# Kernel optimization log

Hardware: AMD Instinct MI355X
Metric: run time of the kernel (lower is better)

Reference implementation:

```python
import jax, jax.numpy as jnp
import numpy as np

N, D, H, E, K = 8192, 1024, 4096, 8, 2


def setup_inputs() -> dict:
    key = jax.random.key(0)
    ks = jax.random.split(key, 4)
    scaled = lambda k, shp, fan: (jax.random.normal(k, shp, jnp.float32) / np.sqrt(fan).astype(np.float32))
    return {
        "x": jax.random.normal(ks[0], (N, D), jnp.float32),
        "Wg": scaled(ks[1], (D, E), D),
        "bg": jnp.zeros((E,), jnp.float32),
        "W1": scaled(ks[2], (E, D, H), D),
        "b1": jnp.zeros((E, H), jnp.float32),
        "W2": scaled(ks[3], (E, H, D), H),
        "b2": jnp.zeros((E, D), jnp.float32),
    }


def reference(x, Wg, bg, W1, b1, W2, b2):
    # Gating: softmax over experts, top-k selection, renormalize top-k probs.
    gate_probs = jax.nn.softmax(x @ Wg + bg, axis=-1)            # [N, E]
    topk_p, topk_i = jax.lax.top_k(gate_probs, K)                # [N, K]
    topk_p = topk_p / topk_p.sum(axis=-1, keepdims=True)
    onehot = jax.nn.one_hot(topk_i, E, dtype=x.dtype)            # [N, K, E]
    # Per-token combine weight for each expert (0 if expert not in top-k).
    w = (onehot * topk_p[..., None]).sum(axis=1)                 # [N, E]

    out = jnp.zeros_like(x)
    for e in range(E):  # fixed small loop over structurally distinct experts
        h = jax.nn.relu(x @ W1[e] + b1[e])                       # dropout = identity (eval)
        out = out + w[:, e:e + 1] * (h @ W2[e] + b2[e])

    # Load-balancing auxiliary loss.
    importance = gate_probs.sum(axis=0)
    importance = importance / importance.sum()
    load = onehot.sum(axis=(0, 1)) / (x.shape[0] * K)            # [E]
    lb_loss = E * (importance * load).sum()
    return out, lb_loss
```

## Files before the change

kernel.cpp:

```cpp
#include <hip/hip_runtime.h>
#include <hip/hip_bf16.h>
#include <math.h>

#define NTOK 8192
#define DDIM 1024
#define HDIM 4096
#define NEXP 8
#define KTOP 2
#define MAXROWS 17408
#define MAXTILES 136

typedef __bf16 bf16x8 __attribute__((ext_vector_type(8)));
typedef float f32x4 __attribute__((ext_vector_type(4)));

#define GAS __attribute__((address_space(1)))
#define LAS __attribute__((address_space(3)))

__device__ __forceinline__ void async16(const void* g, void* l) {
  __builtin_amdgcn_global_load_lds((GAS void*)g, (LAS void*)l, 16, 0, 0);
}

#define XB_OFF     ((size_t)0)
#define W1T_OFF    (XB_OFF + (size_t)NTOK*DDIM*2)
#define ROWOUT_OFF W1T_OFF
#define W2T_OFF    (W1T_OFF + (size_t)NEXP*DDIM*HDIM*2)
#define HB_OFF     (W2T_OFF + (size_t)NEXP*HDIM*DDIM*2)
#define ROWTOK_OFF (HB_OFF + (size_t)MAXROWS*HDIM*2)
#define ROWW_OFF   (ROWTOK_OFF + (size_t)MAXROWS*4)
#define TOKE_OFF   (ROWW_OFF + (size_t)MAXROWS*4)
#define TOKW_OFF   (TOKE_OFF + (size_t)NTOK*KTOP*4)
#define TOKROW_OFF (TOKW_OFF + (size_t)NTOK*KTOP*4)
#define TILEE_OFF  (TOKROW_OFF + (size_t)NTOK*KTOP*4)
#define CNT_OFF    (TILEE_OFF + (size_t)256*4)
#define POS_OFF    (CNT_OFF + 64)
#define IMP_OFF    (POS_OFF + 64)
#define META_OFF   (IMP_OFF + 64)

__global__ void init_kernel(int* counts, float* importance) {
  if (threadIdx.x < NEXP) { counts[threadIdx.x] = 0; importance[threadIdx.x] = 0.f; }
}

__global__ void cast_x_kernel(const float* __restrict__ src, __hip_bfloat16* __restrict__ dst) {
  size_t i = ((size_t)blockIdx.x * blockDim.x + threadIdx.x) * 4;
  if (i < (size_t)NTOK * DDIM) {
    float4 v = *(const float4*)(src + i);
    dst[i + 0] = __float2bfloat16(v.x);
    dst[i + 1] = __float2bfloat16(v.y);
    dst[i + 2] = __float2bfloat16(v.z);
    dst[i + 3] = __float2bfloat16(v.w);
  }
}

__global__ __launch_bounds__(256) void transpose_cast_kernel(
    const float* __restrict__ src, __hip_bfloat16* __restrict__ dst, int R, int C) {
  __shared__ float tile[64][65];
  const int e = blockIdx.z;
  const float* s = src + (size_t)e * R * C;
  __hip_bfloat16* d = dst + (size_t)e * R * C;
  const int c0 = blockIdx.x * 64, r0 = blockIdx.y * 64;
  const int tc = (threadIdx.x & 15) * 4;
  const int tr = threadIdx.x >> 4;
#pragma unroll
  for (int p = 0; p < 4; ++p) {
    float4 v = *(const float4*)&s[(size_t)(r0 + tr + p * 16) * C + c0 + tc];
    tile[tr + p * 16][tc + 0] = v.x;
    tile[tr + p * 16][tc + 1] = v.y;
    tile[tr + p * 16][tc + 2] = v.z;
    tile[tr + p * 16][tc + 3] = v.w;
  }
  __syncthreads();
  const int oc = threadIdx.x >> 4;
  const int orr = (threadIdx.x & 15) * 4;
#pragma unroll
  for (int p = 0; p < 4; ++p) {
    const int c = oc + p * 16;
    __hip_bfloat16 tmp[4];
    tmp[0] = __float2bfloat16(tile[orr + 0][c]);
    tmp[1] = __float2bfloat16(tile[orr + 1][c]);
    tmp[2] = __float2bfloat16(tile[orr + 2][c]);
    tmp[3] = __float2bfloat16(tile[orr + 3][c]);
    *(ushort4*)&d[(size_t)(c0 + c) * R + r0 + orr] = *(ushort4*)tmp;
  }
}

__global__ __launch_bounds__(256) void gating_kernel(
    const float* __restrict__ x, const float* __restrict__ Wg, const float* __restrict__ bg,
    int* __restrict__ tok_e, float* __restrict__ tok_w,
    int* __restrict__ counts, float* __restrict__ importance) {
  const int tid = threadIdx.x, wid = tid >> 6, lane = tid & 63;
  const int t = blockIdx.x * 32 + wid * 8 + (lane >> 3);
  const int e = lane & 7;
  const float* xr = x + (size_t)t * DDIM;
  double dot = 0.0;
  for (int d = 0; d < DDIM; d += 4) {
    float4 xv = *(const float4*)(xr + d);
    dot += (double)xv.x * (double)Wg[(d + 0) * NEXP + e];
    dot += (double)xv.y * (double)Wg[(d + 1) * NEXP + e];
    dot += (double)xv.z * (double)Wg[(d + 2) * NEXP + e];
    dot += (double)xv.w * (double)Wg[(d + 3) * NEXP + e];
  }
  double logit = dot + (double)bg[e];
  double m = logit;
  for (int off = 1; off < 8; off <<= 1) {
    double o = __shfl_xor(m, off, 64);
    m = o > m ? o : m;
  }
  double p = exp(logit - m);
  double s = p;
  for (int off = 1; off < 8; off <<= 1) s += __shfl_xor(s, off, 64);
  float prob = (float)(p / s);

  __shared__ float imp[NEXP];
  __shared__ int cnt[NEXP];
  if (tid < NEXP) { imp[tid] = 0.f; cnt[tid] = 0; }
  __syncthreads();
  atomicAdd(&imp[e], prob);

  float bp = prob; int be = e;
  for (int off = 1; off < 8; off <<= 1) {
    float op = __shfl_xor(bp, off, 64); int oe = __shfl_xor(be, off, 64);
    if (op > bp || (op == bp && oe < be)) { bp = op; be = oe; }
  }
  float p2 = (e == be) ? -1.f : prob;
  float sp = p2; int se = e;
  for (int off = 1; off < 8; off <<= 1) {
    float op = __shfl_xor(sp, off, 64); int oe = __shfl_xor(se, off, 64);
    if (op > sp || (op == sp && oe < se)) { sp = op; se = oe; }
  }
  if (e == 0) {
    float tsum = bp + sp;
    tok_e[t * 2 + 0] = be; tok_e[t * 2 + 1] = se;
    tok_w[t * 2 + 0] = bp / tsum; tok_w[t * 2 + 1] = sp / tsum;
    atomicAdd(&cnt[be], 1); atomicAdd(&cnt[se], 1);
  }
  __syncthreads();
  if (tid < NEXP) {
    atomicAdd(&counts[tid], cnt[tid]);
    atomicAdd(&importance[tid], imp[tid]);
  }
}

__global__ void offsets_kernel(const int* __restrict__ counts, int* pos, int* tile_expert,
                               int* meta, int* row_token) {
  if (threadIdx.x == 0) {
    int pb = 0, tb = 0;
    for (int e = 0; e < NEXP; e++) {
      pos[e] = pb;
      int tiles = (counts[e] + 127) >> 7;
      for (int tt = 0; tt < tiles; ++tt) tile_expert[tb + tt] = e;
      pb += tiles * 128; tb += tiles;
    }
    meta[0] = tb;
  }
  __syncthreads();
  for (int i = threadIdx.x; i < MAXROWS; i += blockDim.x) row_token[i] = -1;
}

__global__ void scatter_kernel(const int* __restrict__ tok_e, const float* __restrict__ tok_w,
                               int* __restrict__ pos, int* __restrict__ row_token,
                               float* __restrict__ row_weight, int* __restrict__ tok_row) {
  __shared__ int lcnt[NEXP], lbase[NEXP];
  const int t = blockIdx.x * 256 + threadIdx.x;
  if (threadIdx.x < NEXP) lcnt[threadIdx.x] = 0;
  __syncthreads();
  const int e0 = tok_e[t * 2 + 0], e1 = tok_e[t * 2 + 1];
  const int s0 = atomicAdd(&lcnt[e0], 1);
  const int s1 = atomicAdd(&lcnt[e1], 1);
  __syncthreads();
  if (threadIdx.x < NEXP) lbase[threadIdx.x] = atomicAdd(&pos[threadIdx.x], lcnt[threadIdx.x]);
  __syncthreads();
  int r0 = lbase[e0] + s0; row_token[r0] = t; row_weight[r0] = tok_w[t * 2 + 0]; tok_row[t * 2 + 0] = r0;
  int r1 = lbase[e1] + s1; row_token[r1] = t; row_weight[r1] = tok_w[t * 2 + 1]; tok_row[t * 2 + 1] = r1;
}

__global__ __launch_bounds__(256) void gemm1_kernel(
    const __hip_bfloat16* __restrict__ xb, const __hip_bfloat16* __restrict__ w1t,
    const float* __restrict__ b1, __hip_bfloat16* __restrict__ hb,
    const int* __restrict__ row_token, const int* __restrict__ tile_expert,
    const int* __restrict__ meta) {
  const int tile_y = blockIdx.y;
  if (tile_y >= meta[0]) return;
  const int n0 = blockIdx.x * 128;
  const int e = tile_expert[tile_y];
  const int r0 = tile_y * 128;
  const int tid = threadIdx.x;
  const int wid = tid >> 6, lane = tid & 63;

  __shared__ __align__(16) __hip_bfloat16 As[2][128 * 32];
  __shared__ __align__(16) __hip_bfloat16 Bs[2][128 * 32];

  const int srow = wid * 32 + (lane >> 2);
  const int g = (((lane & 3) - (srow & 3) - ((srow >> 2) & 3)) & 3) * 8;
  int t0 = row_token[r0 + srow];      if (t0 < 0) t0 = 0;
  int t1 = row_token[r0 + srow + 16]; if (t1 < 0) t1 = 0;
  const __hip_bfloat16* ga0 = xb + (size_t)t0 * DDIM + g;
  const __hip_bfloat16* ga1 = xb + (size_t)t1 * DDIM + g;
  const __hip_bfloat16* gb0 = w1t + ((size_t)e * HDIM + n0 + srow) * DDIM + g;
  const __hip_bfloat16* gb1 = gb0 + (size_t)16 * DDIM;
  const int ldsA0 = (wid * 32) * 32, ldsA1 = (wid * 32 + 16) * 32;

  f32x4 acc[4][4] = {};
  const int wm = (wid & 1) * 64, wn = (wid >> 1) * 64;
  const int fr = lane & 15;
  const int soff = (((lane >> 4) + (lane & 3) + ((lane >> 2) & 3)) & 3) * 8;

#define STAGE1(b) do { \
    async16(ga0, &As[b][ldsA0]); async16(ga1, &As[b][ldsA1]); \
    async16(gb0, &Bs[b][ldsA0]); async16(gb1, &Bs[b][ldsA1]); \
    ga0 += 32; ga1 += 32; gb0 += 32; gb1 += 32; } while (0)

  STAGE1(0);
  for (int kt = 0; kt < DDIM / 32; ++kt) {
    const int cur = kt & 1;
    __syncthreads();
    if (kt + 1 < DDIM / 32) { if (cur) STAGE1(0); else STAGE1(1); }
    bf16x8 av[4], bv[4];
#pragma unroll
    for (int i = 0; i < 4; i++) av[i] = *(const bf16x8*)&As[cur][(wm + i * 16 + fr) * 32 + soff];
#pragma unroll
    for (int j = 0; j < 4; j++) bv[j] = *(const bf16x8*)&Bs[cur][(wn + j * 16 + fr) * 32 + soff];
#pragma unroll
    for (int i = 0; i < 4; i++)
#pragma unroll
      for (int j = 0; j < 4; j++)
        acc[i][j] = __builtin_amdgcn_mfma_f32_16x16x32_bf16(av[i], bv[j], acc[i][j], 0, 0, 0);
  }
#undef STAGE1

  const int crow = (lane >> 4) * 4;
  const int ccol = lane & 15;
#pragma unroll
  for (int j = 0; j < 4; j++) {
    const int gc = n0 + wn + j * 16 + ccol;
    const float bias = b1[e * HDIM + gc];
#pragma unroll
    for (int i = 0; i < 4; i++) {
      const int grb = r0 + wm + i * 16 + crow;
#pragma unroll
      for (int r = 0; r < 4; r++) {
        float v = acc[i][j][r] + bias;
        v = v > 0.f ? v : 0.f;
        hb[(size_t)(grb + r) * HDIM + gc] = __float2bfloat16(v);
      }
    }
  }
}

__global__ __launch_bounds__(256) void gemm2_kernel(
    const __hip_bfloat16* __restrict__ hb, const __hip_bfloat16* __restrict__ w2t,
    const float* __restrict__ b2, __hip_bfloat16* __restrict__ rowout,
    const int* __restrict__ tile_expert, const int* __restrict__ meta) {
  const int tile_y = blockIdx.x >> 3;
  const int cx = blockIdx.x & 7;
  if (tile_y >= meta[0]) return;
  const int n0 = cx * 128;
  const int e = tile_expert[tile_y];
  const int r0 = tile_y * 128;
  const int tid = threadIdx.x;
  const int wid = tid >> 6, lane = tid & 63;

  __shared__ __align__(16) __hip_bfloat16 As[2][128 * 32];
  __shared__ __align__(16) __hip_bfloat16 Bs[2][128 * 32];

  const int srow = wid * 32 + (lane >> 2);
  const int g = (((lane & 3) - (srow & 3) - ((srow >> 2) & 3)) & 3) * 8;
  const __hip_bfloat16* ga0 = hb + ((size_t)r0 + srow) * HDIM + g;
  const __hip_bfloat16* ga1 = ga0 + (size_t)16 * HDIM;
  const __hip_bfloat16* gb0 = w2t + ((size_t)e * DDIM + n0 + srow) * HDIM + g;
  const __hip_bfloat16* gb1 = gb0 + (size_t)16 * HDIM;
  const int ldsA0 = (wid * 32) * 32, ldsA1 = (wid * 32 + 16) * 32;

  f32x4 acc[4][4] = {};
  const int wm = (wid & 1) * 64, wn = (wid >> 1) * 64;
  const int fr = lane & 15;
  const int soff = (((lane >> 4) + (lane & 3) + ((lane >> 2) & 3)) & 3) * 8;

#define STAGE2(b) do { \
    async16(ga0, &As[b][ldsA0]); async16(ga1, &As[b][ldsA1]); \
    async16(gb0, &Bs[b][ldsA0]); async16(gb1, &Bs[b][ldsA1]); \
    ga0 += 32; ga1 += 32; gb0 += 32; gb1 += 32; } while (0)

  STAGE2(0);
  for (int kt = 0; kt < HDIM / 32; ++kt) {
    const int cur = kt & 1;
    __syncthreads();
    if (kt + 1 < HDIM / 32) { if (cur) STAGE2(0); else STAGE2(1); }
    bf16x8 av[4], bv[4];
#pragma unroll
    for (int i = 0; i < 4; i++) av[i] = *(const bf16x8*)&As[cur][(wm + i * 16 + fr) * 32 + soff];
#pragma unroll
    for (int j = 0; j < 4; j++) bv[j] = *(const bf16x8*)&Bs[cur][(wn + j * 16 + fr) * 32 + soff];
#pragma unroll
    for (int i = 0; i < 4; i++)
#pragma unroll
      for (int j = 0; j < 4; j++)
        acc[i][j] = __builtin_amdgcn_mfma_f32_16x16x32_bf16(av[i], bv[j], acc[i][j], 0, 0, 0);
  }
#undef STAGE2

  const int crow = (lane >> 4) * 4;
  const int ccol = lane & 15;
#pragma unroll
  for (int j = 0; j < 4; j++) {
    const int gc = n0 + wn + j * 16 + ccol;
    const float bias = b2[e * DDIM + gc];
#pragma unroll
    for (int i = 0; i < 4; i++) {
      const int rr = r0 + wm + i * 16 + crow;
#pragma unroll
      for (int r = 0; r < 4; r++)
        rowout[(size_t)(rr + r) * DDIM + gc] = __float2bfloat16(acc[i][j][r] + bias);
    }
  }
}

__global__ __launch_bounds__(256) void combine_kernel(
    const __hip_bfloat16* __restrict__ rowout, const int* __restrict__ tok_row,
    const float* __restrict__ row_weight, float* __restrict__ out) {
  const int idx = blockIdx.x * 256 + threadIdx.x;
  const int t = idx >> 7;
  const int d = (idx & 127) * 8;
  const int r0 = tok_row[t * 2 + 0], r1 = tok_row[t * 2 + 1];
  const float w0 = row_weight[r0], w1 = row_weight[r1];
  bf16x8 a = *(const bf16x8*)&rowout[(size_t)r0 * DDIM + d];
  bf16x8 b = *(const bf16x8*)&rowout[(size_t)r1 * DDIM + d];
  float o[8];
#pragma unroll
  for (int k = 0; k < 8; k++) o[k] = w0 * (float)a[k] + w1 * (float)b[k];
  float* dst = out + (size_t)t * DDIM + d;
  *(float4*)(dst + 0) = make_float4(o[0], o[1], o[2], o[3]);
  *(float4*)(dst + 4) = make_float4(o[4], o[5], o[6], o[7]);
}

__global__ void finalize_kernel(const float* __restrict__ importance,
                                const int* __restrict__ counts, float* __restrict__ lb_out) {
  if (threadIdx.x == 0 && blockIdx.x == 0) {
    float s = 0.f;
    for (int e = 0; e < NEXP; e++) s += importance[e];
    float lb = 0.f;
    for (int e = 0; e < NEXP; e++)
      lb += (importance[e] / s) * ((float)counts[e] / (float)(NTOK * KTOP));
    lb_out[0] = (float)NEXP * lb;
  }
}

extern "C" void kernel_launch(void* const* d_in, const int* in_sizes, int n_in,
                              void* d_out, int out_size, void* d_ws, size_t ws_size,
                              hipStream_t stream) {
  (void)in_sizes; (void)n_in; (void)out_size; (void)ws_size;
  const float* x  = (const float*)d_in[0];
  const float* Wg = (const float*)d_in[1];
  const float* bg = (const float*)d_in[2];
  const float* W1 = (const float*)d_in[3];
  const float* b1 = (const float*)d_in[4];
  const float* W2 = (const float*)d_in[5];
  const float* b2 = (const float*)d_in[6];
  float* out = (float*)d_out;

  char* ws = (char*)d_ws;
  __hip_bfloat16* xb     = (__hip_bfloat16*)(ws + XB_OFF);
  __hip_bfloat16* w1t    = (__hip_bfloat16*)(ws + W1T_OFF);
  __hip_bfloat16* rowout = (__hip_bfloat16*)(ws + ROWOUT_OFF);
  __hip_bfloat16* w2t    = (__hip_bfloat16*)(ws + W2T_OFF);
  __hip_bfloat16* hb     = (__hip_bfloat16*)(ws + HB_OFF);
  int*   row_token  = (int*)(ws + ROWTOK_OFF);
  float* row_weight = (float*)(ws + ROWW_OFF);
  int*   tok_e   = (int*)(ws + TOKE_OFF);
  float* tok_w   = (float*)(ws + TOKW_OFF);
  int*   tok_row = (int*)(ws + TOKROW_OFF);
  int*   tile_e  = (int*)(ws + TILEE_OFF);
  int*   counts  = (int*)(ws + CNT_OFF);
  int*   pos     = (int*)(ws + POS_OFF);
  float* importance = (float*)(ws + IMP_OFF);
  int*   meta    = (int*)(ws + META_OFF);

  init_kernel<<<1, 64, 0, stream>>>(counts, importance);
  cast_x_kernel<<<NTOK * DDIM / 4 / 256, 256, 0, stream>>>(x, xb);
  transpose_cast_kernel<<<dim3(HDIM / 64, DDIM / 64, NEXP), 256, 0, stream>>>(W1, w1t, DDIM, HDIM);
  transpose_cast_kernel<<<dim3(DDIM / 64, HDIM / 64, NEXP), 256, 0, stream>>>(W2, w2t, HDIM, DDIM);
  gating_kernel<<<NTOK / 32, 256, 0, stream>>>(x, Wg, bg, tok_e, tok_w, counts, importance);
  offsets_kernel<<<1, 256, 0, stream>>>(counts, pos, tile_e, meta, row_token);
  scatter_kernel<<<NTOK / 256, 256, 0, stream>>>(tok_e, tok_w, pos, row_token, row_weight, tok_row);
  gemm1_kernel<<<dim3(HDIM / 128, MAXTILES), 256, 0, stream>>>(xb, w1t, b1, hb, row_token, tile_e, meta);
  gemm2_kernel<<<dim3((DDIM / 128) * MAXTILES), 256, 0, stream>>>(hb, w2t, b2, rowout, tile_e, meta);
  combine_kernel<<<NTOK * 128 / 256, 256, 0, stream>>>(rowout, tok_row, row_weight, out);
  finalize_kernel<<<1, 64, 0, stream>>>(importance, counts, out + (size_t)NTOK * DDIM);
}
```

Baseline: 800.2 us.

## Use 64x256 expert tiles and merge both MoE GEMMs into one template

Routing tiles shrink from 128 to 64 rows per expert, which cuts padding waste in the grouped rows. The GEMM block tile changes from 128x128 to 64x256, with each wave owning 64 columns and all 64 rows. The two GEMM kernels become one templated kernel with gather and ReLU flags, and both use a 1D grid ordered row-tile-major. The change trades lower padding and more B reuse against less A reuse per block and different L2 behaviour.

```diff
diff --git a/kernel.cpp b/kernel.cpp
--- a/kernel.cpp
+++ b/kernel.cpp
@@ -7,8 +7,8 @@
 #define HDIM 4096
 #define NEXP 8
 #define KTOP 2
-#define MAXROWS 17408
-#define MAXTILES 136
+#define MAXROWS 16896
+#define MAXTILES 264
 
 typedef __bf16 bf16x8 __attribute__((ext_vector_type(8)));
 typedef float f32x4 __attribute__((ext_vector_type(4)));
@@ -31,7 +31,7 @@
 #define TOKW_OFF   (TOKE_OFF + (size_t)NTOK*KTOP*4)
 #define TOKROW_OFF (TOKW_OFF + (size_t)NTOK*KTOP*4)
 #define TILEE_OFF  (TOKROW_OFF + (size_t)NTOK*KTOP*4)
-#define CNT_OFF    (TILEE_OFF + (size_t)256*4)
+#define CNT_OFF    (TILEE_OFF + (size_t)512*4)
 #define POS_OFF    (CNT_OFF + 64)
 #define IMP_OFF    (POS_OFF + 64)
 #define META_OFF   (IMP_OFF + 64)
@@ -146,9 +146,9 @@
     int pb = 0, tb = 0;
     for (int e = 0; e < NEXP; e++) {
       pos[e] = pb;
-      int tiles = (counts[e] + 127) >> 7;
+      int tiles = (counts[e] + 63) >> 6;
       for (int tt = 0; tt < tiles; ++tt) tile_expert[tb + tt] = e;
-      pb += tiles * 128; tb += tiles;
+      pb += tiles * 64; tb += tiles;
     }
     meta[0] = tb;
   }
@@ -173,50 +173,63 @@
   int r1 = lbase[e1] + s1; row_token[r1] = t; row_weight[r1] = tok_w[t * 2 + 1]; tok_row[t * 2 + 1] = r1;
 }
 
-__global__ __launch_bounds__(256) void gemm1_kernel(
-    const __hip_bfloat16* __restrict__ xb, const __hip_bfloat16* __restrict__ w1t,
-    const float* __restrict__ b1, __hip_bfloat16* __restrict__ hb,
+template<int NDIM, int KDIM, bool GATHER, bool RELU>
+__global__ __launch_bounds__(256) void moe_gemm_kernel(
+    const __hip_bfloat16* __restrict__ Ag, const __hip_bfloat16* __restrict__ Bg,
+    const float* __restrict__ bias, __hip_bfloat16* __restrict__ Cg,
     const int* __restrict__ row_token, const int* __restrict__ tile_expert,
     const int* __restrict__ meta) {
-  const int tile_y = blockIdx.y;
-  if (tile_y >= meta[0]) return;
-  const int n0 = blockIdx.x * 128;
-  const int e = tile_expert[tile_y];
-  const int r0 = tile_y * 128;
+  const int NCOLT = NDIM / 256;
+  const int ty = blockIdx.x / NCOLT;
+  const int cx = blockIdx.x % NCOLT;
+  if (ty >= meta[0]) return;
+  const int e = tile_expert[ty];
+  const int r0 = ty * 64;
+  const int n0 = cx * 256;
   const int tid = threadIdx.x;
   const int wid = tid >> 6, lane = tid & 63;
 
-  __shared__ __align__(16) __hip_bfloat16 As[2][128 * 32];
-  __shared__ __align__(16) __hip_bfloat16 Bs[2][128 * 32];
-
-  const int srow = wid * 32 + (lane >> 2);
-  const int g = (((lane & 3) - (srow & 3) - ((srow >> 2) & 3)) & 3) * 8;
-  int t0 = row_token[r0 + srow];      if (t0 < 0) t0 = 0;
-  int t1 = row_token[r0 + srow + 16]; if (t1 < 0) t1 = 0;
-  const __hip_bfloat16* ga0 = xb + (size_t)t0 * DDIM + g;
-  const __hip_bfloat16* ga1 = xb + (size_t)t1 * DDIM + g;
-  const __hip_bfloat16* gb0 = w1t + ((size_t)e * HDIM + n0 + srow) * DDIM + g;
-  const __hip_bfloat16* gb1 = gb0 + (size_t)16 * DDIM;
-  const int ldsA0 = (wid * 32) * 32, ldsA1 = (wid * 32 + 16) * 32;
+  __shared__ __align__(16) __hip_bfloat16 As[2][64 * 32];
+  __shared__ __align__(16) __hip_bfloat16 Bs[2][256 * 32];
+
+  const int g = (((lane & 3) - ((lane >> 2) & 3) - (lane >> 4)) & 3) * 8;
+  const int srl = lane >> 2;
+  const __hip_bfloat16* ga;
+  if (GATHER) {
+    int t = row_token[r0 + wid * 16 + srl]; if (t < 0) t = 0;
+    ga = Ag + (size_t)t * KDIM + g;
+  } else {
+    ga = Ag + (size_t)(r0 + wid * 16 + srl) * KDIM + g;
+  }
+  const __hip_bfloat16* gb[4];
+#pragma unroll
+  for (int c = 0; c < 4; ++c)
+    gb[c] = Bg + ((size_t)e * NDIM + n0 + wid * 64 + c * 16 + srl) * KDIM + g;
+  const int ldsA = wid * 16 * 32;
+  const int ldsB = wid * 64 * 32;
 
   f32x4 acc[4][4] = {};
-  const int wm = (wid & 1) * 64, wn = (wid >> 1) * 64;
+  const int wn = wid * 64;
   const int fr = lane & 15;
   const int soff = (((lane >> 4) + (lane & 3) + ((lane >> 2) & 3)) & 3) * 8;
 
-#define STAGE1(b) do { \
-    async16(ga0, &As[b][ldsA0]); async16(ga1, &As[b][ldsA1]); \
-    async16(gb0, &Bs[b][ldsA0]); async16(gb1, &Bs[b][ldsA1]); \
-    ga0 += 32; ga1 += 32; gb0 += 32; gb1 += 32; } while (0)
-
-  STAGE1(0);
-  for (int kt = 0; kt < DDIM / 32; ++kt) {
+#define STAGE(b) do { \
+    async16(ga, &As[b][ldsA]); \
+    async16(gb[0], &Bs[b][ldsB]); \
+    async16(gb[1], &Bs[b][ldsB + 16 * 32]); \
+    async16(gb[2], &Bs[b][ldsB + 32 * 32]); \
+    async16(gb[3], &Bs[b][ldsB + 48 * 32]); \
+    ga += 32; gb[0] += 32; gb[1] += 32; gb[2] += 32; gb[3] += 32; } while (0)
+
+  STAGE(0);
+  const int NT = KDIM / 32;
+  for (int kt = 0; kt < NT; ++kt) {
     const int cur = kt & 1;
     __syncthreads();
-    if (kt + 1 < DDIM / 32) { if (cur) STAGE1(0); else STAGE1(1); }
+    if (kt + 1 < NT) { if (cur) STAGE(0); else STAGE(1); }
     bf16x8 av[4], bv[4];
 #pragma unroll
-    for (int i = 0; i < 4; i++) av[i] = *(const bf16x8*)&As[cur][(wm + i * 16 + fr) * 32 + soff];
+    for (int i = 0; i < 4; i++) av[i] = *(const bf16x8*)&As[cur][(i * 16 + fr) * 32 + soff];
 #pragma unroll
     for (int j = 0; j < 4; j++) bv[j] = *(const bf16x8*)&Bs[cur][(wn + j * 16 + fr) * 32 + soff];
 #pragma unroll
@@ -225,91 +238,23 @@
       for (int j = 0; j < 4; j++)
         acc[i][j] = __builtin_amdgcn_mfma_f32_16x16x32_bf16(av[i], bv[j], acc[i][j], 0, 0, 0);
   }
-#undef STAGE1
+#undef STAGE
 
   const int crow = (lane >> 4) * 4;
   const int ccol = lane & 15;
 #pragma unroll
   for (int j = 0; j < 4; j++) {
     const int gc = n0 + wn + j * 16 + ccol;
-    const float bias = b1[e * HDIM + gc];
+    const float bb = bias[e * NDIM + gc];
 #pragma unroll
     for (int i = 0; i < 4; i++) {
-      const int grb = r0 + wm + i * 16 + crow;
+      const int grb = r0 + i * 16 + crow;
 #pragma unroll
       for (int r = 0; r < 4; r++) {
-        float v = acc[i][j][r] + bias;
-        v = v > 0.f ? v : 0.f;
-        hb[(size_t)(grb + r) * HDIM + gc] = __float2bfloat16(v);
+        float v = acc[i][j][r] + bb;
+        if (RELU) v = v > 0.f ? v : 0.f;
+        Cg[(size_t)(grb + r) * NDIM + gc] = __float2bfloat16(v);
       }
-    }
-  }
-}
-
-__global__ __launch_bounds__(256) void gemm2_kernel(
-    const __hip_bfloat16* __restrict__ hb, const __hip_bfloat16* __restrict__ w2t,
-    const float* __restrict__ b2, __hip_bfloat16* __restrict__ rowout,
-    const int* __restrict__ tile_expert, const int* __restrict__ meta) {
-  const int tile_y = blockIdx.x >> 3;
-  const int cx = blockIdx.x & 7;
-  if (tile_y >= meta[0]) return;
-  const int n0 = cx * 128;
-  const int e = tile_expert[tile_y];
-  const int r0 = tile_y * 128;
-  const int tid = threadIdx.x;
-  const int wid = tid >> 6, lane = tid & 63;
-
-  __shared__ __align__(16) __hip_bfloat16 As[2][128 * 32];
-  __shared__ __align__(16) __hip_bfloat16 Bs[2][128 * 32];
-
-  const int srow = wid * 32 + (lane >> 2);
-  const int g = (((lane & 3) - (srow & 3) - ((srow >> 2) & 3)) & 3) * 8;
-  const __hip_bfloat16* ga0 = hb + ((size_t)r0 + srow) * HDIM + g;
-  const __hip_bfloat16* ga1 = ga0 + (size_t)16 * HDIM;
-  const __hip_bfloat16* gb0 = w2t + ((size_t)e * DDIM + n0 + srow) * HDIM + g;
-  const __hip_bfloat16* gb1 = gb0 + (size_t)16 * HDIM;
-  const int ldsA0 = (wid * 32) * 32, ldsA1 = (wid * 32 + 16) * 32;
-
-  f32x4 acc[4][4] = {};
-  const int wm = (wid & 1) * 64, wn = (wid >> 1) * 64;
-  const int fr = lane & 15;
-  const int soff = (((lane >> 4) + (lane & 3) + ((lane >> 2) & 3)) & 3) * 8;
-
-#define STAGE2(b) do { \
-    async16(ga0, &As[b][ldsA0]); async16(ga1, &As[b][ldsA1]); \
-    async16(gb0, &Bs[b][ldsA0]); async16(gb1, &Bs[b][ldsA1]); \
-    ga0 += 32; ga1 += 32; gb0 += 32; gb1 += 32; } while (0)
-
-  STAGE2(0);
-  for (int kt = 0; kt < HDIM / 32; ++kt) {
-    const int cur = kt & 1;
-    __syncthreads();
-    if (kt + 1 < HDIM / 32) { if (cur) STAGE2(0); else STAGE2(1); }
-    bf16x8 av[4], bv[4];
-#pragma unroll
-    for (int i = 0; i < 4; i++) av[i] = *(const bf16x8*)&As[cur][(wm + i * 16 + fr) * 32 + soff];
-#pragma unroll
-    for (int j = 0; j < 4; j++) bv[j] = *(const bf16x8*)&Bs[cur][(wn + j * 16 + fr) * 32 + soff];
-#pragma unroll
-    for (int i = 0; i < 4; i++)
-#pragma unroll
-      for (int j = 0; j < 4; j++)
-        acc[i][j] = __builtin_amdgcn_mfma_f32_16x16x32_bf16(av[i], bv[j], acc[i][j], 0, 0, 0);
-  }
-#undef STAGE2
-
-  const int crow = (lane >> 4) * 4;
-  const int ccol = lane & 15;
-#pragma unroll
-  for (int j = 0; j < 4; j++) {
-    const int gc = n0 + wn + j * 16 + ccol;
-    const float bias = b2[e * DDIM + gc];
-#pragma unroll
-    for (int i = 0; i < 4; i++) {
-      const int rr = r0 + wm + i * 16 + crow;
-#pragma unroll
-      for (int r = 0; r < 4; r++)
-        rowout[(size_t)(rr + r) * DDIM + gc] = __float2bfloat16(acc[i][j][r] + bias);
     }
   }
 }
@@ -381,8 +326,10 @@
   gating_kernel<<<NTOK / 32, 256, 0, stream>>>(x, Wg, bg, tok_e, tok_w, counts, importance);
   offsets_kernel<<<1, 256, 0, stream>>>(counts, pos, tile_e, meta, row_token);
   scatter_kernel<<<NTOK / 256, 256, 0, stream>>>(tok_e, tok_w, pos, row_token, row_weight, tok_row);
-  gemm1_kernel<<<dim3(HDIM / 128, MAXTILES), 256, 0, stream>>>(xb, w1t, b1, hb, row_token, tile_e, meta);
-  gemm2_kernel<<<dim3((DDIM / 128) * MAXTILES), 256, 0, stream>>>(hb, w2t, b2, rowout, tile_e, meta);
+  moe_gemm_kernel<HDIM, DDIM, true, true>
+      <<<MAXTILES * (HDIM / 256), 256, 0, stream>>>(xb, w1t, b1, hb, row_token, tile_e, meta);
+  moe_gemm_kernel<DDIM, HDIM, false, false>
+      <<<MAXTILES * (DDIM / 256), 256, 0, stream>>>(hb, w2t, b2, rowout, row_token, tile_e, meta);
   combine_kernel<<<NTOK * 128 / 256, 256, 0, stream>>>(rowout, tok_row, row_weight, out);
   finalize_kernel<<<1, 64, 0, stream>>>(importance, counts, out + (size_t)NTOK * DDIM);
 }
```

After: 840.5 us. +5.0%, slower.

## Triple-buffer LDS in both expert GEMMs with partial vmcnt waits

Applied to the files above, without the earlier changes.

Both grouped GEMM kernels move from double to triple-buffered LDS staging. Each loop iteration waits only for the oldest stage's async global-to-LDS loads (vmcnt(4)) and keeps two stages in flight, replacing the full __syncthreads drain with a plain barrier. The goal is to hide global memory latency behind MFMA work. In exchange LDS use per block rises from 32KB to 48KB, which may reduce occupancy, and correctness now depends on the hand-written waitcnt and barrier ordering.

```diff
diff --git a/kernel.cpp b/kernel.cpp
--- a/kernel.cpp
+++ b/kernel.cpp
@@ -186,8 +186,8 @@
   const int tid = threadIdx.x;
   const int wid = tid >> 6, lane = tid & 63;
 
-  __shared__ __align__(16) __hip_bfloat16 As[2][128 * 32];
-  __shared__ __align__(16) __hip_bfloat16 Bs[2][128 * 32];
+  __shared__ __align__(16) __hip_bfloat16 As[3][128 * 32];
+  __shared__ __align__(16) __hip_bfloat16 Bs[3][128 * 32];
 
   const int srow = wid * 32 + (lane >> 2);
   const int g = (((lane & 3) - (srow & 3) - ((srow >> 2) & 3)) & 3) * 8;
@@ -209,21 +209,26 @@
     async16(gb0, &Bs[b][ldsA0]); async16(gb1, &Bs[b][ldsA1]); \
     ga0 += 32; ga1 += 32; gb0 += 32; gb1 += 32; } while (0)
 
+  const int NT = DDIM / 32;
   STAGE1(0);
-  for (int kt = 0; kt < DDIM / 32; ++kt) {
-    const int cur = kt & 1;
-    __syncthreads();
-    if (kt + 1 < DDIM / 32) { if (cur) STAGE1(0); else STAGE1(1); }
+  STAGE1(1);
+  int bc = 0, bn = 1, bnn = 2;
+  for (int kt = 0; kt < NT; ++kt) {
+    if (kt + 1 < NT) asm volatile("s_waitcnt vmcnt(4)" ::: "memory");
+    else             asm volatile("s_waitcnt vmcnt(0)" ::: "memory");
+    __builtin_amdgcn_s_barrier();
+    if (kt + 2 < NT) STAGE1(bnn);
     bf16x8 av[4], bv[4];
 #pragma unroll
-    for (int i = 0; i < 4; i++) av[i] = *(const bf16x8*)&As[cur][(wm + i * 16 + fr) * 32 + soff];
-#pragma unroll
-    for (int j = 0; j < 4; j++) bv[j] = *(const bf16x8*)&Bs[cur][(wn + j * 16 + fr) * 32 + soff];
+    for (int i = 0; i < 4; i++) av[i] = *(const bf16x8*)&As[bc][(wm + i * 16 + fr) * 32 + soff];
+#pragma unroll
+    for (int j = 0; j < 4; j++) bv[j] = *(const bf16x8*)&Bs[bc][(wn + j * 16 + fr) * 32 + soff];
 #pragma unroll
     for (int i = 0; i < 4; i++)
 #pragma unroll
       for (int j = 0; j < 4; j++)
         acc[i][j] = __builtin_amdgcn_mfma_f32_16x16x32_bf16(av[i], bv[j], acc[i][j], 0, 0, 0);
+    const int tmp = bc; bc = bn; bn = bnn; bnn = tmp;
   }
 #undef STAGE1
 
@@ -259,8 +264,8 @@
   const int tid = threadIdx.x;
   const int wid = tid >> 6, lane = tid & 63;
 
-  __shared__ __align__(16) __hip_bfloat16 As[2][128 * 32];
-  __shared__ __align__(16) __hip_bfloat16 Bs[2][128 * 32];
+  __shared__ __align__(16) __hip_bfloat16 As[3][128 * 32];
+  __shared__ __align__(16) __hip_bfloat16 Bs[3][128 * 32];
 
   const int srow = wid * 32 + (lane >> 2);
   const int g = (((lane & 3) - (srow & 3) - ((srow >> 2) & 3)) & 3) * 8;
@@ -280,21 +285,26 @@
     async16(gb0, &Bs[b][ldsA0]); async16(gb1, &Bs[b][ldsA1]); \
     ga0 += 32; ga1 += 32; gb0 += 32; gb1 += 32; } while (0)
 
+  const int NT = HDIM / 32;
   STAGE2(0);
-  for (int kt = 0; kt < HDIM / 32; ++kt) {
-    const int cur = kt & 1;
-    __syncthreads();
-    if (kt + 1 < HDIM / 32) { if (cur) STAGE2(0); else STAGE2(1); }
+  STAGE2(1);
+  int bc = 0, bn = 1, bnn = 2;
+  for (int kt = 0; kt < NT; ++kt) {
+    if (kt + 1 < NT) asm volatile("s_waitcnt vmcnt(4)" ::: "memory");
+    else             asm volatile("s_waitcnt vmcnt(0)" ::: "memory");
+    __builtin_amdgcn_s_barrier();
+    if (kt + 2 < NT) STAGE2(bnn);
     bf16x8 av[4], bv[4];
 #pragma unroll
-    for (int i = 0; i < 4; i++) av[i] = *(const bf16x8*)&As[cur][(wm + i * 16 + fr) * 32 + soff];
-#pragma unroll
-    for (int j = 0; j < 4; j++) bv[j] = *(const bf16x8*)&Bs[cur][(wn + j * 16 + fr) * 32 + soff];
+    for (int i = 0; i < 4; i++) av[i] = *(const bf16x8*)&As[bc][(wm + i * 16 + fr) * 32 + soff];
+#pragma unroll
+    for (int j = 0; j < 4; j++) bv[j] = *(const bf16x8*)&Bs[bc][(wn + j * 16 + fr) * 32 + soff];
 #pragma unroll
     for (int i = 0; i < 4; i++)
 #pragma unroll
       for (int j = 0; j < 4; j++)
         acc[i][j] = __builtin_amdgcn_mfma_f32_16x16x32_bf16(av[i], bv[j], acc[i][j], 0, 0, 0);
+    const int tmp = bc; bc = bn; bn = bnn; bnn = tmp;
   }
 #undef STAGE2
 
```

New measurement: 846.9 us. 1.06x slower.
